# Performance work log

Hardware: AMD Instinct MI355X
Metric: run time of the kernel (lower is better)

The kernel has to match this reference:

```python
import jax, jax.numpy as jnp
import numpy as np

B, L, D, N, KEEP, HID = 64, 256, 128, 8192, 64, 1024
IN_DIM = D + KEEP * D + 1  # q + packed subset keys + log_count


def setup_inputs() -> dict:
    key = jax.random.key(0)
    ks = jax.random.split(key, 7)
    q = jax.random.normal(ks[0], (N, D), jnp.float32)
    k = jax.random.normal(ks[1], (B, L, D), jnp.float32)
    batch_idx = jax.random.randint(ks[2], (N,), 0, B)
    mask = jax.random.randint(ks[3], (N, L), 0, 2).astype(bool)
    count = jax.random.randint(ks[4], (N,), 0, L)
    W1 = jax.random.normal(ks[5], (IN_DIM, HID), jnp.float32) / np.sqrt(IN_DIM).astype(np.float32)
    b1 = jnp.zeros((HID,), jnp.float32)
    W2 = jax.random.normal(ks[6], (HID, 1), jnp.float32) / np.sqrt(HID).astype(np.float32)
    b2 = jnp.zeros((1,), jnp.float32)
    return dict(q=q, k=k, batch_idx=batch_idx, mask=mask, count=count,
                W1=W1, b1=b1, W2=W2, b2=b2)


def _pack_subset_keys(k, batch_idx, mask):
    # chain_k: [N, L, D] gather of per-chain key blocks
    chain_k = k[batch_idx]
    pos = jnp.arange(L, dtype=jnp.float32)
    # score = L - pos for masked positions, 0 otherwise -> topk picks first KEEP masked positions
    scores = mask.astype(jnp.float32) * (jnp.float32(L) - pos)[None, :]
    top_scores, top_idx = jax.lax.top_k(scores, KEEP)
    picked = top_scores > 0
    sortable = jnp.where(picked, top_idx, L)  # sentinel L for unpicked
    sortable = jnp.sort(sortable, axis=1)     # restore ascending position order
    picked = sortable < L
    safe_idx = jnp.where(picked, sortable, 0)
    packed = jnp.take_along_axis(chain_k, safe_idx[:, :, None], axis=1)  # [N, KEEP, D]
    packed = packed * picked[:, :, None].astype(packed.dtype)
    return packed.reshape(N, KEEP * D)


def reference(q, k, batch_idx, mask, count, W1, b1, W2, b2):
    packed = _pack_subset_keys(k, batch_idx, mask)
    log_count = jnp.log1p(count.astype(q.dtype))[:, None]
    feat = jnp.concatenate([q, packed, log_count], axis=-1)  # [N, IN_DIM]
    h = jax.nn.gelu(feat @ W1 + b1, approximate=False)       # torch GELU = exact erf
    return (h @ W2 + b2).squeeze(-1)                          # [N]
```

## Files before the change

kernel.cpp:

```cpp
#include <hip/hip_runtime.h>
#include <math.h>

#define N_ROWS 8192
#define B_CH   64
#define L_SEQ  256
#define D_DIM  128
#define KEEP   64
#define HID    1024
#define KTOT   8320
#define KTILES 260
#define HTILES 64

#define KOFF   (N_ROWS * D_DIM)
#define ZOFF   (KOFF + B_CH * L_SEQ * D_DIM)
#define BUF_ELEMS (ZOFF + 128)

#define PACK_BLOCKS 256
#define QK_BLOCKS   1537
#define W1T_BLOCKS  2080
#define PREP_GRID   (PACK_BLOCKS + QK_BLOCKS + W1T_BLOCKS)

typedef unsigned short ushort_t;
typedef __attribute__((ext_vector_type(8))) short  short8;
typedef __attribute__((ext_vector_type(4))) float  float4v;

__device__ __forceinline__ ushort_t f2bf(float f) {
    union { float f; unsigned int u; } v; v.f = f;
    unsigned int u = v.u;
    unsigned int r = u + 0x7fffu + ((u >> 16) & 1u);
    return (ushort_t)(r >> 16);
}

__device__ __forceinline__ void glds16(const void* g, void* l) {
    __builtin_amdgcn_global_load_lds(
        (const __attribute__((address_space(1))) unsigned int*)g,
        (__attribute__((address_space(3))) unsigned int*)l,
        16, 0, 0);
}

__global__ void prep(const float* __restrict__ q, const float* __restrict__ k,
                     const float* __restrict__ W1, const int* __restrict__ mask,
                     const int* __restrict__ batch_idx, const int* __restrict__ count,
                     const float* __restrict__ b2,
                     ushort_t* __restrict__ buf, ushort_t* __restrict__ w1f,
                     int* __restrict__ srcLUT, float* __restrict__ logc,
                     float* __restrict__ out) {
    __shared__ __align__(16) char smem[16640];
    const int blk = blockIdx.x;
    const int t = threadIdx.x;

    if (blk < PACK_BLOCKS) {
        const int n0 = blk * 32;
        int* sidx = (int*)smem;
        int* bidx_l = (int*)(smem + 32 * 65 * 4);
        for (int i = t; i < 32 * 65; i += 256) sidx[i] = -1;
        if (t < 32) {
            int n = n0 + t;
            bidx_l[t] = batch_idx[n];
            logc[n] = log1pf((float)count[n]);
            srcLUT[n] = n * D_DIM;
            out[n] = b2[0];
        }
        __syncthreads();
        const int w = t >> 6, l = t & 63;
        const unsigned long long ltm = (1ull << l) - 1ull;
        for (int r = 0; r < 8; ++r) {
            const int lr = w * 8 + r;
            const int* mrow = mask + (size_t)(n0 + lr) * L_SEQ;
            int m0 = mrow[l] != 0;
            int m1 = mrow[64 + l] != 0;
            int m2 = mrow[128 + l] != 0;
            int m3 = mrow[192 + l] != 0;
            unsigned long long b0 = __ballot(m0), b1 = __ballot(m1);
            unsigned long long b2v = __ballot(m2), b3 = __ballot(m3);
            int p1 = (int)__popcll(b0);
            int p2 = p1 + (int)__popcll(b1);
            int p3 = p2 + (int)__popcll(b2v);
            int* row = sidx + lr * 65;
            if (m0) { int rk = (int)__popcll(b0 & ltm);       if (rk < KEEP) row[rk] = l; }
            if (m1) { int rk = p1 + (int)__popcll(b1 & ltm);  if (rk < KEEP) row[rk] = 64 + l; }
            if (m2) { int rk = p2 + (int)__popcll(b2v & ltm); if (rk < KEEP) row[rk] = 128 + l; }
            if (m3) { int rk = p3 + (int)__popcll(b3 & ltm);  if (rk < KEEP) row[rk] = 192 + l; }
        }
        __syncthreads();
        for (int e = t; e < KEEP * 32; e += 256) {
            int j = e >> 5, nl = e & 31;
            int s = sidx[nl * 65 + j];
            srcLUT[(size_t)(j + 1) * N_ROWS + n0 + nl] =
                (s >= 0) ? (KOFF + (bidx_l[nl] * L_SEQ + s) * D_DIM) : ZOFF;
        }

    } else if (blk < PACK_BLOCKS + QK_BLOCKS) {
        int c = (blk - PACK_BLOCKS) * 256 + t;
        if (c >= BUF_ELEMS / 8) return;
        int e = c * 8;
        float4 x0, x1;
        if (e < KOFF) {
            const float4* s = (const float4*)(q + e);
            x0 = s[0]; x1 = s[1];
        } else if (e < ZOFF) {
            const float4* s = (const float4*)(k + (e - KOFF));
            x0 = s[0]; x1 = s[1];
        } else {
            x0 = make_float4(0.f, 0.f, 0.f, 0.f);
            x1 = x0;
        }
        union { ushort_t s[8]; uint4 v; } o;
        o.s[0] = f2bf(x0.x); o.s[1] = f2bf(x0.y); o.s[2] = f2bf(x0.z); o.s[3] = f2bf(x0.w);
        o.s[4] = f2bf(x1.x); o.s[5] = f2bf(x1.y); o.s[6] = f2bf(x1.z); o.s[7] = f2bf(x1.w);
        *(uint4*)(buf + e) = o.v;

    } else {
        const int idx = blk - (PACK_BLOCKS + QK_BLOCKS);
        const int k0 = (idx % 130) * 64, h0 = (idx / 130) * 64;
        float (*tile)[65] = (float(*)[65])smem;
        const int r0 = t >> 4, c4 = (t & 15) * 4;
#pragma unroll
        for (int i = 0; i < 4; ++i) {
            const int r = r0 + i * 16;
            const float4 v = *(const float4*)(W1 + (size_t)(k0 + r) * HID + h0 + c4);
            tile[r][c4 + 0] = v.x; tile[r][c4 + 1] = v.y;
            tile[r][c4 + 2] = v.z; tile[r][c4 + 3] = v.w;
        }
        __syncthreads();
#pragma unroll
        for (int i = 0; i < 2; ++i) {
            int s = i * 256 + t;
            int c = s >> 6, l = s & 63;
            int qt = c >> 2, ht = c & 3;
            int ln = l & 15, quad = l >> 4;
            union { ushort_t sv[8]; uint4 v; } o;
#pragma unroll
            for (int j = 0; j < 8; ++j)
                o.sv[j] = f2bf(tile[qt * 32 + quad * 8 + j][ht * 16 + ln]);
            size_t dst = (((size_t)(h0 / 16 + ht) * KTILES + (k0 / 32 + qt)) * 64 + l) * 8;
            *(uint4*)(w1f + dst) = o.v;
        }
    }
}

__global__ __launch_bounds__(256, 2)
void gemm_mlp(const ushort_t* __restrict__ buf, const ushort_t* __restrict__ w1f,
              const int* __restrict__ srcLUT, const float* __restrict__ logc,
              const float* __restrict__ W1, const float* __restrict__ b1,
              const float* __restrict__ W2, float* __restrict__ out) {
    __shared__ ushort_t As[128 * 128];

    const int t = threadIdx.x;
    const int blkH = blockIdx.x, blkM = blockIdx.y;
    const int wave = t >> 6, lane = t & 63;
    const int wm = wave >> 1, wh = wave & 1;
    const int ln = lane & 15, quad = lane >> 4;

    float4v acc[4][4];
#pragma unroll
    for (int i = 0; i < 4; ++i)
#pragma unroll
        for (int j = 0; j < 4; ++j)
#pragma unroll
            for (int r = 0; r < 4; ++r) acc[i][j][r] = 0.0f;

    const int tr = t >> 4;
    const int pg = (t & 15) ^ tr;
    ushort_t* lA = As + t * 8;
    const int* lutBase = srcLUT + blkM * 128 + tr;

    const ushort_t* bp[4];
#pragma unroll
    for (int ni = 0; ni < 4; ++ni)
        bp[ni] = w1f + ((size_t)(blkH * 8 + wh * 4 + ni) * KTILES * 64 + lane) * 8;

    int offA[8];
#pragma unroll
    for (int i = 0; i < 8; ++i) offA[i] = lutBase[i * 16];

    for (int bi = 0; bi < 65; ++bi) {
#pragma unroll
        for (int i = 0; i < 8; ++i)
            glds16(buf + offA[i] + pg * 8, lA + i * 2048);
        short8 bq[4][4];
#pragma unroll
        for (int kk = 0; kk < 4; ++kk)
#pragma unroll
            for (int ni = 0; ni < 4; ++ni)
                bq[kk][ni] = *(const short8*)(bp[ni] + (size_t)(bi * 4 + kk) * 512);
        int offN[8];
        if (bi < 64) {
#pragma unroll
            for (int i = 0; i < 8; ++i) offN[i] = lutBase[(bi + 1) * N_ROWS + i * 16];
        }
        __syncthreads();
#pragma unroll
        for (int kk = 0; kk < 4; ++kk) {
            short8 af[4];
#pragma unroll
            for (int mi = 0; mi < 4; ++mi) {
                const int row = wm * 64 + mi * 16 + ln;
                const int sl = (kk * 4 + quad) ^ ln;
                af[mi] = *(const short8*)(As + row * 128 + sl * 8);
            }
#pragma unroll
            for (int mi = 0; mi < 4; ++mi)
#pragma unroll
                for (int ni = 0; ni < 4; ++ni)
                    acc[mi][ni] = __builtin_amdgcn_mfma_f32_16x16x32_bf16(
                        af[mi], bq[kk][ni], acc[mi][ni], 0, 0, 0);
        }
        __syncthreads();
#pragma unroll
        for (int i = 0; i < 8; ++i) offA[i] = offN[i];
    }

    const float* w1last = W1 + (size_t)KTOT * HID;
    float w1l[4], b1v[4], w2v[4];
#pragma unroll
    for (int ni = 0; ni < 4; ++ni) {
        int h = blkH * 128 + wh * 64 + ni * 16 + ln;
        w1l[ni] = w1last[h];
        b1v[ni] = b1[h];
        w2v[ni] = W2[h];
    }
    const int nbase = blkM * 128 + wm * 64 + quad * 4;
#pragma unroll
    for (int mi = 0; mi < 4; ++mi) {
#pragma unroll
        for (int rg = 0; rg < 4; ++rg) {
            const int n = nbase + mi * 16 + rg;
            const float lc = logc[n];
            float s = 0.0f;
#pragma unroll
            for (int ni = 0; ni < 4; ++ni) {
                float pre = acc[mi][ni][rg] + lc * w1l[ni] + b1v[ni];
                float hv = 0.5f * pre * (1.0f + erff(pre * 0.70710678118654752f));
                s += hv * w2v[ni];
            }
            s += __shfl_xor(s, 1);
            s += __shfl_xor(s, 2);
            s += __shfl_xor(s, 4);
            s += __shfl_xor(s, 8);
            if (ln == 0) atomicAdd(out + n, s);
        }
    }
}

extern "C" void kernel_launch(void* const* d_in, const int* in_sizes, int n_in,
                              void* d_out, int out_size, void* d_ws, size_t ws_size,
                              hipStream_t stream) {
    const float* q     = (const float*)d_in[0];
    const float* k     = (const float*)d_in[1];
    const int*   bidx  = (const int*)d_in[2];
    const int*   mask  = (const int*)d_in[3];
    const int*   count = (const int*)d_in[4];
    const float* W1    = (const float*)d_in[5];
    const float* b1    = (const float*)d_in[6];
    const float* W2    = (const float*)d_in[7];
    const float* b2    = (const float*)d_in[8];
    float* out = (float*)d_out;

    char* ws = (char*)d_ws;
    ushort_t* buf    = (ushort_t*)(ws);
    ushort_t* w1f    = (ushort_t*)(ws + 6291712);
    int*      srcLUT = (int*)(ws + 6291712 + 17039360);
    float*    logc   = (float*)(ws + 6291712 + 17039360 + 2129920);

    prep<<<PREP_GRID, 256, 0, stream>>>(q, k, W1, mask, bidx, count, b2,
                                        buf, w1f, srcLUT, logc, out);
    gemm_mlp<<<dim3(HID / 128, N_ROWS / 128), 256, 0, stream>>>(
        buf, w1f, srcLUT, logc, W1, b1, W2, out);
}
```

Baseline: 242.2 us.

## Double-buffer A tile in LDS with manual vmcnt waits and setprio

Splits the LDS A tile into two buffers and software-pipelines the GEMM loop so the async global-to-LDS load for the next K block is issued before computing the current one. It replaces __syncthreads with explicit s_waitcnt vmcnt and raw barriers, adds sched_barrier fences, and raises wave priority around the MFMA section. LDS use doubles to 64 KB per block, which may cut occupancy under launch_bounds(256,2). The hand-tuned vmcnt counts are fragile and depend on exactly how many loads are outstanding.

```diff
diff --git a/kernel.cpp b/kernel.cpp
--- a/kernel.cpp
+++ b/kernel.cpp
@@ -37,6 +37,9 @@
         (__attribute__((address_space(3))) unsigned int*)l,
         16, 0, 0);
 }
+
+#define SCHED0() __builtin_amdgcn_sched_barrier(0)
+#define WAITVM(n) do { asm volatile("s_waitcnt vmcnt(" #n ")" ::: "memory"); SCHED0(); } while (0)
 
 __global__ void prep(const float* __restrict__ q, const float* __restrict__ k,
                      const float* __restrict__ W1, const int* __restrict__ mask,
@@ -144,7 +147,8 @@
               const int* __restrict__ srcLUT, const float* __restrict__ logc,
               const float* __restrict__ W1, const float* __restrict__ b1,
               const float* __restrict__ W2, float* __restrict__ out) {
-    __shared__ ushort_t As[128 * 128];
+    __shared__ __align__(16) ushort_t As0[128 * 128];
+    __shared__ __align__(16) ushort_t As1[128 * 128];
 
     const int t = threadIdx.x;
     const int blkH = blockIdx.x, blkM = blockIdx.y;
@@ -162,7 +166,8 @@
 
     const int tr = t >> 4;
     const int pg = (t & 15) ^ tr;
-    ushort_t* lA = As + t * 8;
+    ushort_t* lA0 = As0 + t * 8;
+    ushort_t* lA1 = As1 + t * 8;
     const int* lutBase = srcLUT + blkM * 128 + tr;
 
     const ushort_t* bp[4];
@@ -170,26 +175,120 @@
     for (int ni = 0; ni < 4; ++ni)
         bp[ni] = w1f + ((size_t)(blkH * 8 + wh * 4 + ni) * KTILES * 64 + lane) * 8;
 
-    int offA[8];
-#pragma unroll
-    for (int i = 0; i < 8; ++i) offA[i] = lutBase[i * 16];
-
-    for (int bi = 0; bi < 65; ++bi) {
-#pragma unroll
-        for (int i = 0; i < 8; ++i)
-            glds16(buf + offA[i] + pg * 8, lA + i * 2048);
+    int offE[8], offO[8];
+
+    {
+        int offP[8];
+#pragma unroll
+        for (int i = 0; i < 8; ++i) offP[i] = lutBase[i * 16];
+#pragma unroll
+        for (int i = 0; i < 8; ++i) glds16(buf + offP[i] + pg * 8, lA0 + i * 2048);
+#pragma unroll
+        for (int i = 0; i < 8; ++i) offO[i] = lutBase[(size_t)N_ROWS + i * 16];
+        SCHED0();
+    }
+
+#pragma unroll 1
+    for (int m = 0; m < 32; ++m) {
+        {
+            short8 bq[4][4];
+#pragma unroll
+            for (int kk = 0; kk < 4; ++kk)
+#pragma unroll
+                for (int ni = 0; ni < 4; ++ni)
+                    bq[kk][ni] = *(const short8*)(bp[ni] + (size_t)(2 * m * 4 + kk) * 512);
+            SCHED0();
+#pragma unroll
+            for (int i = 0; i < 8; ++i)
+                offE[i] = lutBase[(size_t)(2 * m + 2) * N_ROWS + i * 16];
+            SCHED0();
+#pragma unroll
+            for (int i = 0; i < 8; ++i)
+                glds16(buf + offO[i] + pg * 8, lA1 + i * 2048);
+            SCHED0();
+            WAITVM(32);
+            __builtin_amdgcn_s_barrier();
+            SCHED0();
+            __builtin_amdgcn_s_setprio(1);
+#pragma unroll
+            for (int kk = 0; kk < 4; ++kk) {
+                short8 af[4];
+#pragma unroll
+                for (int mi = 0; mi < 4; ++mi) {
+                    const int row = wm * 64 + mi * 16 + ln;
+                    const int sl = (kk * 4 + quad) ^ ln;
+                    af[mi] = *(const short8*)(As0 + row * 128 + sl * 8);
+                }
+#pragma unroll
+                for (int mi = 0; mi < 4; ++mi)
+#pragma unroll
+                    for (int ni = 0; ni < 4; ++ni)
+                        acc[mi][ni] = __builtin_amdgcn_mfma_f32_16x16x32_bf16(
+                            af[mi], bq[kk][ni], acc[mi][ni], 0, 0, 0);
+            }
+            __builtin_amdgcn_s_setprio(0);
+            SCHED0();
+            __builtin_amdgcn_s_barrier();
+            SCHED0();
+        }
+
+        {
+            short8 bq[4][4];
+#pragma unroll
+            for (int kk = 0; kk < 4; ++kk)
+#pragma unroll
+                for (int ni = 0; ni < 4; ++ni)
+                    bq[kk][ni] = *(const short8*)(bp[ni] + (size_t)((2 * m + 1) * 4 + kk) * 512);
+            SCHED0();
+            const int tl = (2 * m + 3 > 64) ? 64 : (2 * m + 3);
+#pragma unroll
+            for (int i = 0; i < 8; ++i)
+                offO[i] = lutBase[(size_t)tl * N_ROWS + i * 16];
+            SCHED0();
+#pragma unroll
+            for (int i = 0; i < 8; ++i)
+                glds16(buf + offE[i] + pg * 8, lA0 + i * 2048);
+            SCHED0();
+            WAITVM(32);
+            __builtin_amdgcn_s_barrier();
+            SCHED0();
+            __builtin_amdgcn_s_setprio(1);
+#pragma unroll
+            for (int kk = 0; kk < 4; ++kk) {
+                short8 af[4];
+#pragma unroll
+                for (int mi = 0; mi < 4; ++mi) {
+                    const int row = wm * 64 + mi * 16 + ln;
+                    const int sl = (kk * 4 + quad) ^ ln;
+                    af[mi] = *(const short8*)(As1 + row * 128 + sl * 8);
+                }
+#pragma unroll
+                for (int mi = 0; mi < 4; ++mi)
+#pragma unroll
+                    for (int ni = 0; ni < 4; ++ni)
+                        acc[mi][ni] = __builtin_amdgcn_mfma_f32_16x16x32_bf16(
+                            af[mi], bq[kk][ni], acc[mi][ni], 0, 0, 0);
+            }
+            __builtin_amdgcn_s_setprio(0);
+            SCHED0();
+            __builtin_amdgcn_s_barrier();
+            SCHED0();
+        }
+    }
+#pragma unroll
+    for (int i = 0; i < 8; ++i) asm volatile("" :: "v"(offO[i]));
+
+    {
         short8 bq[4][4];
 #pragma unroll
         for (int kk = 0; kk < 4; ++kk)
 #pragma unroll
             for (int ni = 0; ni < 4; ++ni)
-                bq[kk][ni] = *(const short8*)(bp[ni] + (size_t)(bi * 4 + kk) * 512);
-        int offN[8];
-        if (bi < 64) {
-#pragma unroll
-            for (int i = 0; i < 8; ++i) offN[i] = lutBase[(bi + 1) * N_ROWS + i * 16];
-        }
-        __syncthreads();
+                bq[kk][ni] = *(const short8*)(bp[ni] + (size_t)(64 * 4 + kk) * 512);
+        SCHED0();
+        WAITVM(0);
+        __builtin_amdgcn_s_barrier();
+        SCHED0();
 #pragma unroll
         for (int kk = 0; kk < 4; ++kk) {
             short8 af[4];
@@ -197,7 +296,7 @@
             for (int mi = 0; mi < 4; ++mi) {
                 const int row = wm * 64 + mi * 16 + ln;
                 const int sl = (kk * 4 + quad) ^ ln;
-                af[mi] = *(const short8*)(As + row * 128 + sl * 8);
+                af[mi] = *(const short8*)(As0 + row * 128 + sl * 8);
             }
 #pragma unroll
             for (int mi = 0; mi < 4; ++mi)
@@ -206,9 +305,6 @@
                     acc[mi][ni] = __builtin_amdgcn_mfma_f32_16x16x32_bf16(
                         af[mi], bq[kk][ni], acc[mi][ni], 0, 0, 0);
         }
-        __syncthreads();
-#pragma unroll
-        for (int i = 0; i < 8; ++i) offA[i] = offN[i];
     }
 
     const float* w1last = W1 + (size_t)KTOT * HID;
```

Result: slower. 267.4 us (+10.4%).
